# Optimization experiments

Measured on AMD Instinct MI355X. Metric: run time of the kernel, lower is better.

## Reference

```python
import jax, jax.numpy as jnp
import numpy as np

V, C, S, H, B, T = 10000, 1024, 128, 256, 16, 128
NEG = -1e10


def _mlp(x, w1, b1, w2, b2, wo, bo):
    # ResidualLayer (dropout=0, eval): relu(lin1) -> relu(lin2 + residual), then final Linear
    h = jax.nn.relu(x @ w1 + b1)
    h = jax.nn.relu(h @ w2 + b2 + x)
    return h @ wo + bo


def setup_inputs() -> dict:
    key = jax.random.key(0)
    ks = iter(jax.random.split(key, 32))
    d = {}
    d["text"] = jax.random.randint(next(ks), (B, T), 0, V)
    d["word2state"] = jax.random.randint(next(ks), (V, S), 0, C)

    def rn(shape, scale):
        return jax.random.normal(next(ks), shape, dtype=jnp.float32) * scale

    s = 1.0 / np.sqrt(H)
    d["start_emb"] = rn((C, H), 1.0)
    d["start_w1"], d["start_b1"] = rn((H, H), s), jnp.zeros((H,), jnp.float32)
    d["start_w2"], d["start_b2"] = rn((H, H), s), jnp.zeros((H,), jnp.float32)
    d["start_wo"], d["start_bo"] = rn((H, 1), s), jnp.zeros((1,), jnp.float32)
    d["state_emb"] = rn((C, H), 1.0)
    d["trans_w1"], d["trans_b1"] = rn((H, H), s), jnp.zeros((H,), jnp.float32)
    d["trans_w2"], d["trans_b2"] = rn((H, H), s), jnp.zeros((H,), jnp.float32)
    d["trans_wo"], d["trans_bo"] = rn((H, C), s), jnp.zeros((C,), jnp.float32)
    d["pre_emb"] = rn((C, H), 1.0)
    d["term_w1"], d["term_b1"] = rn((H, H), s), jnp.zeros((H,), jnp.float32)
    d["term_w2"], d["term_b2"] = rn((H, H), s), jnp.zeros((H,), jnp.float32)
    d["term_wo"], d["term_bo"] = rn((H, V), s), jnp.zeros((V,), jnp.float32)
    return d


def _evidence(text, word2state,
              start_emb, start_w1, start_b1, start_w2, start_b2, start_wo, start_bo,
              state_emb, trans_w1, trans_b1, trans_w2, trans_b2, trans_wo, trans_bo,
              pre_emb, term_w1, term_b1, term_w2, term_b2, term_wo, term_bo):
    # start distribution over C states
    start = jax.nn.log_softmax(
        _mlp(start_emb, start_w1, start_b1, start_w2, start_b2, start_wo, start_bo)[:, 0])
    # transition [C, C]
    transition = jax.nn.log_softmax(
        _mlp(state_emb, trans_w1, trans_b1, trans_w2, trans_b2, trans_wo, trans_bo), axis=-1)
    # emission with sparse state->word mask (scatter of word2state)
    em_logits = _mlp(pre_emb, term_w1, term_b1, term_w2, term_b2, term_wo, term_bo)  # [C, V]
    a = jnp.repeat(jnp.arange(V), S)  # word index per (word, slot)
    mask = jnp.zeros((C, V), dtype=bool).at[word2state.reshape(-1), a].set(True)
    emission = jax.nn.log_softmax(jnp.where(mask, em_logits, NEG), axis=-1)  # [C, V]

    clamped = word2state[text]  # [B, T, S] states allowed per token
    init = start[clamped[:, 0]]  # [B, S]
    # transition restricted to clamped states: [B, T-1, S_prev, S_next]
    lp = transition[clamped[:, :-1, :, None], clamped[:, 1:, None, :]]
    obs = emission[clamped, text[:, :, None]]  # [B, T, S]
    lp = lp + obs[:, 1:, None, :]                     # emission of next token
    lp = lp.at[:, 0].add(init[:, :, None] + obs[:, 0, :, None])
    lp = jnp.swapaxes(lp, -1, -2)  # [B, T-1, S_next, S_prev]

    # forward algorithm (log-space scan)
    alpha = jax.nn.logsumexp(lp[:, 0], axis=-1)  # [B, S]
    pots = jnp.swapaxes(lp[:, 1:], 0, 1)  # [T-2, B, S, S]

    def step(a_prev, pot):
        return jax.nn.logsumexp(pot + a_prev[:, None, :], axis=-1), None

    alpha_T, _ = jax.lax.scan(step, alpha, pots)
    return jax.nn.logsumexp(alpha_T, axis=-1).sum()


def reference(text, word2state,
              start_emb, start_w1, start_b1, start_w2, start_b2, start_wo, start_bo,
              state_emb, trans_w1, trans_b1, trans_w2, trans_b2, trans_wo, trans_bo,
              pre_emb, term_w1, term_b1, term_w2, term_b2, term_wo, term_bo):
    return _evidence(text, word2state,
                     start_emb, start_w1, start_b1, start_w2, start_b2, start_wo, start_bo,
                     state_emb, trans_w1, trans_b1, trans_w2, trans_b2, trans_wo, trans_bo,
                     pre_emb, term_w1, term_b1, term_w2, term_b2, term_wo, term_bo)
```

## Files before the change

### kernel.cpp

```cpp
#include <hip/hip_runtime.h>
#include <hip/hip_bf16.h>

#define V 10000
#define VP 10112
#define C 1024
#define S 128
#define H 256
#define B 16
#define T 128
#define NR 64
#define CHUNK 158
#define LDK 40

typedef unsigned short u16;
typedef unsigned int u32;
typedef __bf16 bf16x8 __attribute__((ext_vector_type(8)));
typedef float f32x4 __attribute__((ext_vector_type(4)));

static __device__ __forceinline__ float bf2f(u16 x){ return __uint_as_float(((u32)x)<<16); }
static __device__ __forceinline__ u16 f2bf(float f){ u32 u=__float_as_uint(f); return (u16)((u + 0x7FFFu + ((u>>16)&1u))>>16); }

struct Cvt3 { const float* s0; const float* s1; const float* s2; u16* d0; u16* d1; u16* d2; };
__global__ __launch_bounds__(256) void k_cvt3(Cvt3 a){
  const float* s = (blockIdx.y==0)? a.s0 : (blockIdx.y==1)? a.s1 : a.s2;
  u16* d = (blockIdx.y==0)? a.d0 : (blockIdx.y==1)? a.d1 : a.d2;
  int i = (blockIdx.x*256 + threadIdx.x)*8;
  float4 x0 = *(const float4*)(s+i);
  float4 x1 = *(const float4*)(s+i+4);
  u16 h[8] = {f2bf(x0.x),f2bf(x0.y),f2bf(x0.z),f2bf(x0.w),f2bf(x1.x),f2bf(x1.y),f2bf(x1.z),f2bf(x1.w)};
  *(uint4*)(d+i) = *(uint4*)h;
}

__global__ __launch_bounds__(256) void k_transpose(const float* __restrict__ src, u16* __restrict__ dst, int N){
  __shared__ float tile[32][33];
  int v0 = blockIdx.x*32, k0 = blockIdx.y*32;
  int tx = threadIdx.x, ty = threadIdx.y;
  for (int i=0;i<32;i+=8){
    int k = k0+ty+i, v = v0+tx;
    tile[ty+i][tx] = (v < N) ? src[(size_t)k*N + v] : 0.f;
  }
  __syncthreads();
  for (int i=0;i<32;i+=8){
    int v = v0+ty+i, k = k0+tx;
    dst[(size_t)v*H + k] = f2bf(tile[tx][ty+i]);
  }
}

struct T6 { const float* s[6]; u16* d[6]; };
__global__ __launch_bounds__(256) void k_transpose6(T6 a){
  const float* src = a.s[blockIdx.z];
  u16* dst = a.d[blockIdx.z];
  __shared__ float tile[32][33];
  int v0 = blockIdx.x*32, k0 = blockIdx.y*32;
  int tx = threadIdx.x, ty = threadIdx.y;
  for (int i=0;i<32;i+=8){
    int k = k0+ty+i, v = v0+tx;
    tile[ty+i][tx] = src[(size_t)k*H + v];
  }
  __syncthreads();
  for (int i=0;i<32;i+=8){
    int v = v0+ty+i, k = k0+tx;
    dst[(size_t)v*H + k] = f2bf(tile[tx][ty+i]);
  }
}

struct M3 { const u16* A[3]; const u16* W[3]; const float* bias[3]; const u16* R[3]; u16* O[3]; };
template<int RESID>
__global__ __launch_bounds__(256) void k_mlpg(M3 a){
  const int z = blockIdx.z;
  const u16* A  = a.A[z];
  const u16* BT = a.W[z];
  const float* bias = a.bias[z];
  const u16* Rm = a.R[z];
  u16* O = a.O[z];
  __shared__ u16 As[128*LDK];
  __shared__ u16 Bs[128*LDK];
  const int tid = threadIdx.x;
  const int lane = tid & 63, wave = tid >> 6;
  const int wm = wave >> 1, wn = wave & 1;
  const int m0 = blockIdx.y * 128, n0 = blockIdx.x * 128;
  const int lr = lane & 15, lg = lane >> 4;
  f32x4 acc[4][4] = {};
  const int sr = tid >> 1, sh = (tid & 1) * 16;
  for (int ks = 0; ks < H; ks += 32){
    const u16* ga = A  + (size_t)(m0 + sr)*H + ks + sh;
    const u16* gb = BT + (size_t)(n0 + sr)*H + ks + sh;
    uint4 a0 = *(const uint4*)ga;
    uint4 a1 = *(const uint4*)(ga + 8);
    uint4 b0 = *(const uint4*)gb;
    uint4 b1 = *(const uint4*)(gb + 8);
    __syncthreads();
    *(uint4*)&As[sr*LDK + sh]     = a0;
    *(uint4*)&As[sr*LDK + sh + 8] = a1;
    *(uint4*)&Bs[sr*LDK + sh]     = b0;
    *(uint4*)&Bs[sr*LDK + sh + 8] = b1;
    __syncthreads();
    bf16x8 af[4], bfr[4];
    #pragma unroll
    for (int m=0;m<4;m++) af[m]  = *(const bf16x8*)&As[(wm*64 + m*16 + lr)*LDK + lg*8];
    #pragma unroll
    for (int n=0;n<4;n++) bfr[n] = *(const bf16x8*)&Bs[(wn*64 + n*16 + lr)*LDK + lg*8];
    #pragma unroll
    for (int m=0;m<4;m++)
      #pragma unroll
      for (int n=0;n<4;n++)
        acc[m][n] = __builtin_amdgcn_mfma_f32_16x16x32_bf16(af[m], bfr[n], acc[m][n], 0,0,0);
  }
  #pragma unroll
  for (int m=0;m<4;m++){
    int r_g = m0 + wm*64 + m*16 + lg*4;
    #pragma unroll
    for (int n=0;n<4;n++){
      int n_g = n0 + wn*64 + n*16 + lr;
      float bv = bias[n_g];
      #pragma unroll
      for (int reg=0; reg<4; reg++){
        int r = r_g + reg;
        float val = acc[m][n][reg] + bv;
        if (RESID) val += bf2f(Rm[(size_t)r*H + n_g]);
        val = fmaxf(val, 0.f);
        O[(size_t)r*H + n_g] = f2bf(val);
      }
    }
  }
}

__global__ __launch_bounds__(1024) void k_start(
    const u16* __restrict__ h2, const float* __restrict__ wo, const float* __restrict__ bo,
    float* __restrict__ start_lp){
  const int c = threadIdx.x;
  const int lane = c & 63, wid = c >> 6;
  __shared__ float red[16];
  __shared__ float Ms, Zs;
  float acc = bo[0];
  const u16* row = h2 + (size_t)c*H;
  for (int k=0;k<H;k+=8){
    uint4 hv = *(const uint4*)(row+k);
    float4 w0 = *(const float4*)(wo+k);
    float4 w1 = *(const float4*)(wo+k+4);
    acc = fmaf(bf2f((u16)(hv.x&0xFFFFu)), w0.x, acc);
    acc = fmaf(bf2f((u16)(hv.x>>16)),     w0.y, acc);
    acc = fmaf(bf2f((u16)(hv.y&0xFFFFu)), w0.z, acc);
    acc = fmaf(bf2f((u16)(hv.y>>16)),     w0.w, acc);
    acc = fmaf(bf2f((u16)(hv.z&0xFFFFu)), w1.x, acc);
    acc = fmaf(bf2f((u16)(hv.z>>16)),     w1.y, acc);
    acc = fmaf(bf2f((u16)(hv.w&0xFFFFu)), w1.z, acc);
    acc = fmaf(bf2f((u16)(hv.w>>16)),     w1.w, acc);
  }
  float m = acc;
  for (int o=1;o<64;o<<=1) m = fmaxf(m, __shfl_xor(m,o));
  if (lane==0) red[wid]=m;
  __syncthreads();
  if (c==0){ float t=red[0]; for(int i=1;i<16;i++) t=fmaxf(t,red[i]); Ms=t; }
  __syncthreads();
  float M = Ms;
  float e = expf(acc - M);
  float sum = e;
  for (int o=1;o<64;o<<=1) sum += __shfl_xor(sum,o);
  __syncthreads();
  if (lane==0) red[wid]=sum;
  __syncthreads();
  if (c==0){ float t=0.f; for(int i=0;i<16;i++) t+=red[i]; Zs=t; }
  __syncthreads();
  start_lp[c] = acc - (M + logf(Zs));
}

template<int BIAS_ROW, int BF16OUT>
__global__ __launch_bounds__(256) void k_gemm(
    const u16* __restrict__ A, const u16* __restrict__ BT,
    const float* __restrict__ bias, int biasBound,
    void* __restrict__ outp, int ldout){
  __shared__ u16 As[128*LDK];
  __shared__ u16 Bs[128*LDK];
  const int tid = threadIdx.x;
  const int lane = tid & 63, wave = tid >> 6;
  const int wm = wave >> 1, wn = wave & 1;
  const int m0 = blockIdx.y * 128, n0 = blockIdx.x * 128;
  const int lr = lane & 15, lg = lane >> 4;
  f32x4 acc[4][4] = {};
  const int sr = tid >> 1, sh = (tid & 1) * 16;
  for (int ks = 0; ks < H; ks += 32){
    const u16* ga = A  + (size_t)(m0 + sr)*H + ks + sh;
    const u16* gb = BT + (size_t)(n0 + sr)*H + ks + sh;
    uint4 a0 = *(const uint4*)ga;
    uint4 a1 = *(const uint4*)(ga + 8);
    uint4 b0 = *(const uint4*)gb;
    uint4 b1 = *(const uint4*)(gb + 8);
    __syncthreads();
    *(uint4*)&As[sr*LDK + sh]     = a0;
    *(uint4*)&As[sr*LDK + sh + 8] = a1;
    *(uint4*)&Bs[sr*LDK + sh]     = b0;
    *(uint4*)&Bs[sr*LDK + sh + 8] = b1;
    __syncthreads();
    bf16x8 af[4], bfr[4];
    #pragma unroll
    for (int m=0;m<4;m++) af[m]  = *(const bf16x8*)&As[(wm*64 + m*16 + lr)*LDK + lg*8];
    #pragma unroll
    for (int n=0;n<4;n++) bfr[n] = *(const bf16x8*)&Bs[(wn*64 + n*16 + lr)*LDK + lg*8];
    #pragma unroll
    for (int m=0;m<4;m++)
      #pragma unroll
      for (int n=0;n<4;n++)
        acc[m][n] = __builtin_amdgcn_mfma_f32_16x16x32_bf16(af[m], bfr[n], acc[m][n], 0,0,0);
  }
  #pragma unroll
  for (int m=0;m<4;m++){
    int r_g = m0 + wm*64 + m*16 + lg*4;
    #pragma unroll
    for (int n=0;n<4;n++){
      int n_g = n0 + wn*64 + n*16 + lr;
      float bcol = BIAS_ROW ? 0.f : bias[n_g];
      #pragma unroll
      for (int reg=0; reg<4; reg++){
        int r = r_g + reg;
        float bv = BIAS_ROW ? ((r < biasBound) ? bias[r] : 0.f) : bcol;
        float val = acc[m][n][reg] + bv;
        if (BF16OUT) ((u16*)outp)[(size_t)r*ldout + n_g] = f2bf(val);
        else         ((float*)outp)[(size_t)r*ldout + n_g] = val;
      }
    }
  }
}

__global__ __launch_bounds__(256) void k_softmax(const float* __restrict__ TL, u16* __restrict__ P){
  const int c = blockIdx.x;
  const int tid = threadIdx.x, lane = tid & 63, wid = tid >> 6;
  __shared__ float red[4];
  __shared__ float Ms, Zs;
  float4 v = ((const float4*)(TL + (size_t)c*C))[tid];
  float m = fmaxf(fmaxf(v.x,v.y), fmaxf(v.z,v.w));
  for (int o=1;o<64;o<<=1) m = fmaxf(m, __shfl_xor(m,o));
  if (lane==0) red[wid] = m;
  __syncthreads();
  if (tid==0) Ms = fmaxf(fmaxf(red[0],red[1]), fmaxf(red[2],red[3]));
  __syncthreads();
  float M = Ms;
  float e0 = expf(v.x-M), e1 = expf(v.y-M), e2 = expf(v.z-M), e3 = expf(v.w-M);
  float s = (e0+e1)+(e2+e3);
  for (int o=1;o<64;o<<=1) s += __shfl_xor(s,o);
  if (lane==0) red[wid] = s;
  __syncthreads();
  if (tid==0) Zs = red[0]+red[1]+red[2]+red[3];
  __syncthreads();
  float inv = 1.f/Zs;
  u32 lo = (u32)f2bf(e0*inv) | ((u32)f2bf(e1*inv)<<16);
  u32 hi = (u32)f2bf(e2*inv) | ((u32)f2bf(e3*inv)<<16);
  *(uint2*)(P + (size_t)c*C + tid*4) = make_uint2(lo, hi);
}

__global__ __launch_bounds__(256) void k_colmax(const u16* __restrict__ EM, float* __restrict__ shiftp){
  const int c = blockIdx.x*256 + threadIdx.x;
  const int v0 = blockIdx.y*CHUNK;
  float m = -1e30f;
  const u16* p = EM + (size_t)v0*C + c;
  #pragma unroll 2
  for (int i=0;i<CHUNK;i++){ m = fmaxf(m, bf2f(p[0])); p += C; }
  shiftp[(size_t)blockIdx.y*C + c] = m;
}

__global__ void k_shiftc(const float* __restrict__ shiftp, float* __restrict__ shift){
  int c = threadIdx.x + blockIdx.x*blockDim.x;
  if (c < C){
    float m = -1e30f;
    for (int r=0;r<NR;r++) m = fmaxf(m, shiftp[(size_t)r*C + c]);
    shift[c] = m;
  }
}

__global__ __launch_bounds__(256) void k_scatter(
    const int* __restrict__ w2s, const u16* __restrict__ EM,
    const float* __restrict__ shift, u16* __restrict__ D){
  int idx = blockIdx.x*256 + threadIdx.x;
  int v = idx >> 7;
  const int c = w2s[idx];
  float val = bf2f(EM[(size_t)v*C + c]);
  D[(size_t)v*C + c] = f2bf(expf(val - shift[c]));
}

__global__ __launch_bounds__(256) void k_colsum(const u16* __restrict__ D, float* __restrict__ sumexp){
  const int c = blockIdx.x*256 + threadIdx.x;
  const int v0 = blockIdx.y*CHUNK;
  float s = 0.f;
  const u16* p = D + (size_t)v0*C + c;
  #pragma unroll 2
  for (int i=0;i<CHUNK;i++){ s += bf2f(p[0]); p += C; }
  sumexp[(size_t)blockIdx.y*C + c] = s;
}

__global__ void k_lse(const float* __restrict__ shift, const float* __restrict__ sumexp, float* __restrict__ lse){
  int c = threadIdx.x + blockIdx.x*blockDim.x;
  if (c < C){
    float s = 0.f;
    for (int r=0;r<NR;r++) s += sumexp[(size_t)r*C + c];
    lse[c] = shift[c] + logf(s);
  }
}

__global__ __launch_bounds__(128) void k_obs(
    const int* __restrict__ text, const int* __restrict__ w2s,
    const u16* __restrict__ EM, const float* __restrict__ lse,
    float* __restrict__ obs){
  const int bt = blockIdx.x;
  const int s = threadIdx.x;
  const int v = text[bt];
  const int c = w2s[(size_t)v*S + s];
  obs[(size_t)bt*S + s] = bf2f(EM[(size_t)v*C + c]) - lse[c];
}

__global__ __launch_bounds__(256) void k_pot(
    const int* __restrict__ text, const int* __restrict__ w2s,
    const float* __restrict__ start_lp, const float* __restrict__ obs,
    const u16* __restrict__ P, u16* __restrict__ pot){
  const int t = blockIdx.x;
  const int b = blockIdx.y;
  const int tid = threadIdx.x;
  u16* dst = pot + ((size_t)b*128 + t)*(S*S);
  if (t == 127){
    #pragma unroll
    for (int k=0;k<8;k++){
      int e0 = (k*256 + tid)*8;
      int row = e0>>7, c0 = e0&127;
      union { uint4 w; u16 h[8]; } u;
      u.w = make_uint4(0,0,0,0);
      int d = row - c0;
      if (d >= 0 && d < 8) u.h[d] = 0x3F80u;
      *(uint4*)(dst + e0) = u.w;
    }
    return;
  }
  __shared__ int cp[S], cn[S];
  __shared__ float eo[S];
  __shared__ float a0[S];
  __shared__ u32 tileW[S*65];
  u16* tile16 = (u16*)tileW;
  if (tid < 128){
    int cpv = w2s[(size_t)text[b*T + t]*S + tid];
    cp[tid] = cpv;
    a0[tid] = (t==0) ? expf(start_lp[cpv] + obs[(size_t)(b*T)*S + tid]) : 1.0f;
    eo[tid] = expf(obs[((size_t)b*T + t + 1)*S + tid]);
  } else {
    cn[tid-128] = w2s[(size_t)text[b*T + t+1]*S + (tid-128)];
  }
  __syncthreads();
  const int sp_half = tid >> 7;
  const int sn = tid & 127;
  const int cnv = cn[sn];
  const float eov = eo[sn];
  for (int it=0; it<64; ++it){
    int sp = it*2 + sp_half;
    tile16[sn*130 + sp] = f2bf(bf2f(P[(size_t)cp[sp]*C + cnv]) * eov * a0[sp]);
  }
  __syncthreads();
  if (t & 1){
    #pragma unroll
    for (int ii=0; ii<8; ++ii){
      int i0 = (ii*256 + tid)*8;
      int sn2 = i0>>7, sp2 = i0&127;
      const u32* tw = tileW + sn2*65 + (sp2>>1);
      uint4 w4; w4.x = tw[0]; w4.y = tw[1]; w4.z = tw[2]; w4.w = tw[3];
      *(uint4*)(dst + i0) = w4;
    }
  } else {
    #pragma unroll
    for (int ii=0; ii<8; ++ii){
      int i0 = (ii*256 + tid)*8;
      int sp2 = i0>>7, sn0 = i0&127;
      union { uint4 w; u16 h[8]; } u;
      #pragma unroll
      for (int j=0;j<8;j++) u.h[j] = tile16[(sn0+j)*130 + sp2];
      *(uint4*)(dst + i0) = u.w;
    }
  }
}

__global__ __launch_bounds__(256) void k_pair(
    const u16* __restrict__ in, u16* __restrict__ out,
    float* __restrict__ scales, int nin, int soff){
  const int j = blockIdx.x;
  const int b = blockIdx.y;
  const int nout = nin >> 1;
  const u16* Ag = in + ((size_t)b*nin + 2*j+1)*(S*S);
  const u16* Bg = in + ((size_t)b*nin + 2*j  )*(S*S);
  u16* Cg = out + ((size_t)b*nout + j)*(S*S);
  const int tid = threadIdx.x;
  const int lane = tid & 63, wave = tid >> 6;
  const int wm = wave >> 1, wn = wave & 1;
  const int lr = lane & 15, lg = lane >> 4;
  f32x4 acc[4][4] = {};
  #pragma unroll
  for (int kc=0; kc<4; ++kc){
    bf16x8 af[4], bfr[4];
    #pragma unroll
    for (int m=0;m<4;m++) af[m]  = *(const bf16x8*)(Ag + (size_t)(wm*64+m*16+lr)*128 + kc*32 + lg*8);
    #pragma unroll
    for (int n=0;n<4;n++) bfr[n] = *(const bf16x8*)(Bg + (size_t)(wn*64+n*16+lr)*128 + kc*32 + lg*8);
    #pragma unroll
    for (int m=0;m<4;m++)
      #pragma unroll
      for (int n=0;n<4;n++)
        acc[m][n] = __builtin_amdgcn_mfma_f32_16x16x32_bf16(af[m], bfr[n], acc[m][n], 0,0,0);
  }
  __shared__ float red[4];
  float mx = 0.f;
  #pragma unroll
  for (int m=0;m<4;m++)
    #pragma unroll
    for (int n=0;n<4;n++)
      #pragma unroll
      for (int r=0;r<4;r++) mx = fmaxf(mx, acc[m][n][r]);
  for (int o=1;o<64;o<<=1) mx = fmaxf(mx, __shfl_xor(mx,o));
  if (lane==0) red[wave] = mx;
  __syncthreads();
  mx = fmaxf(fmaxf(red[0],red[1]), fmaxf(red[2],red[3]));
  const float sc = 1.0f / mx;
  if (tid==0) scales[(size_t)b*127 + soff + j] = logf(mx);
  if (j & 1){
    #pragma unroll
    for (int m=0;m<4;m++){
      int rg = wm*64 + m*16 + lg*4;
      #pragma unroll
      for (int n=0;n<4;n++){
        int cg = wn*64 + n*16 + lr;
        #pragma unroll
        for (int r=0;r<4;r++) Cg[(size_t)(rg+r)*128 + cg] = f2bf(acc[m][n][r]*sc);
      }
    }
  } else {
    #pragma unroll
    for (int m=0;m<4;m++){
      int rg = wm*64 + m*16 + lg*4;
      #pragma unroll
      for (int n=0;n<4;n++){
        int cg = wn*64 + n*16 + lr;
        float v0=acc[m][n][0]*sc, v1=acc[m][n][1]*sc, v2=acc[m][n][2]*sc, v3=acc[m][n][3]*sc;
        u32 p0, p1;
        asm("v_cvt_pk_bf16_f32 %0, %1, %2" : "=v"(p0) : "v"(v0), "v"(v1));
        asm("v_cvt_pk_bf16_f32 %0, %1, %2" : "=v"(p1) : "v"(v2), "v"(v3));
        *(uint2*)(Cg + (size_t)cg*128 + rg) = make_uint2(p0, p1);
      }
    }
  }
}

__global__ __launch_bounds__(256) void k_fin(
    const u16* __restrict__ fin, const float* __restrict__ scales, float* __restrict__ res){
  const int b = blockIdx.x;
  const int tid = threadIdx.x, lane = tid & 63, wid = tid >> 6;
  __shared__ float red[8];
  const u16* p = fin + (size_t)b*(S*S);
  float s = 0.f;
  #pragma unroll
  for (int i=0;i<8;i++){
    uint4 w = *(const uint4*)(p + (i*256+tid)*8);
    s += bf2f((u16)(w.x&0xFFFFu)) + bf2f((u16)(w.x>>16))
       + bf2f((u16)(w.y&0xFFFFu)) + bf2f((u16)(w.y>>16))
       + bf2f((u16)(w.z&0xFFFFu)) + bf2f((u16)(w.z>>16))
       + bf2f((u16)(w.w&0xFFFFu)) + bf2f((u16)(w.w>>16));
  }
  for (int o=1;o<64;o<<=1) s += __shfl_xor(s,o);
  if (lane==0) red[wid] = s;
  float sl = (tid < 127) ? scales[(size_t)b*127 + tid] : 0.f;
  for (int o=1;o<64;o<<=1) sl += __shfl_xor(sl,o);
  if (lane==0) red[4+wid] = sl;
  __syncthreads();
  if (tid==0){
    float tot = red[0]+red[1]+red[2]+red[3];
    float ssum = red[4]+red[5]+red[6]+red[7];
    res[b] = logf(tot) + ssum;
  }
}

__global__ void k_final(const float* __restrict__ res, float* __restrict__ out){
  if (threadIdx.x==0){
    float s = 0.f;
    for (int i=0;i<B;i++) s += res[i];
    out[0] = s;
  }
}

extern "C" void kernel_launch(void* const* d_in, const int* in_sizes, int n_in,
                              void* d_out, int out_size, void* d_ws, size_t ws_size,
                              hipStream_t stream){
  const int*   text      = (const int*)d_in[0];
  const int*   w2s       = (const int*)d_in[1];
  const float* start_emb = (const float*)d_in[2];
  const float* start_w1  = (const float*)d_in[3];
  const float* start_b1  = (const float*)d_in[4];
  const float* start_w2  = (const float*)d_in[5];
  const float* start_b2  = (const float*)d_in[6];
  const float* start_wo  = (const float*)d_in[7];
  const float* start_bo  = (const float*)d_in[8];
  const float* state_emb = (const float*)d_in[9];
  const float* trans_w1  = (const float*)d_in[10];
  const float* trans_b1  = (const float*)d_in[11];
  const float* trans_w2  = (const float*)d_in[12];
  const float* trans_b2  = (const float*)d_in[13];
  const float* trans_wo  = (const float*)d_in[14];
  const float* trans_bo  = (const float*)d_in[15];
  const float* pre_emb   = (const float*)d_in[16];
  const float* term_w1   = (const float*)d_in[17];
  const float* term_b1   = (const float*)d_in[18];
  const float* term_w2   = (const float*)d_in[19];
  const float* term_b2   = (const float*)d_in[20];
  const float* term_wo   = (const float*)d_in[21];
  const float* term_bo   = (const float*)d_in[22];

  char* ws = (char*)d_ws;
  size_t off = 0;
  auto alloc = [&](size_t bytes)->char*{ char* p = ws + off; off += (bytes + 255) & ~(size_t)255; return p; };
  u16*   embb     = (u16*)  alloc(sizeof(u16)*3*(size_t)C*H);
  u16*   h1b      = (u16*)  alloc(sizeof(u16)*3*(size_t)C*H);
  u16*   h2b      = (u16*)  alloc(sizeof(u16)*3*(size_t)C*H);
  u16*   wt       = (u16*)  alloc(sizeof(u16)*6*(size_t)H*H);
  float* start_lp = (float*)alloc(sizeof(float)*C);
  float* shift    = (float*)alloc(sizeof(float)*C);
  float* shiftp   = (float*)alloc(sizeof(float)*(size_t)C*NR);
  float* sumexp   = (float*)alloc(sizeof(float)*(size_t)C*NR);
  float* lse      = (float*)alloc(sizeof(float)*C);
  float* resb     = (float*)alloc(sizeof(float)*B);
  float* scales   = (float*)alloc(sizeof(float)*(size_t)B*127);
  u16*   P        = (u16*)  alloc(sizeof(u16)*(size_t)C*C);
  u16*   wotb     = (u16*)  alloc(sizeof(u16)*(size_t)VP*H);
  u16*   wottr    = (u16*)  alloc(sizeof(u16)*(size_t)C*H);
  float* obs      = (float*)alloc(sizeof(float)*(size_t)B*T*S);
  u16*   potS     = (u16*)  alloc(sizeof(u16)*(size_t)B*128*S*S);
  u16*   treeA    = (u16*)  alloc(sizeof(u16)*(size_t)B*64*S*S);
  u16*   treeB    = (u16*)  alloc(sizeof(u16)*(size_t)B*32*S*S);
  u16*   EM       = (u16*)potS;
  float* TL       = (float*)treeA;
  u16*   D        = (u16*)((char*)treeA + sizeof(float)*(size_t)C*C);
  (void)ws_size; (void)in_sizes; (void)n_in; (void)out_size;

  u16* embb0 = embb, *embb1 = embb + (size_t)C*H, *embb2 = embb + 2*(size_t)C*H;
  u16* h1b0 = h1b, *h1b1 = h1b + (size_t)C*H, *h1b2 = h1b + 2*(size_t)C*H;
  u16* h2b0 = h2b, *h2b1 = h2b + (size_t)C*H, *h2b2 = h2b + 2*(size_t)C*H;

  hipMemsetAsync(D, 0, sizeof(u16)*(size_t)VP*C, stream);

  Cvt3 cv; cv.s0 = start_emb; cv.s1 = state_emb; cv.s2 = pre_emb;
  cv.d0 = embb0; cv.d1 = embb1; cv.d2 = embb2;
  k_cvt3<<<dim3(C*H/(256*8), 3), dim3(256), 0, stream>>>(cv);

  T6 t6;
  t6.s[0]=start_w1; t6.s[1]=start_w2; t6.s[2]=trans_w1; t6.s[3]=trans_w2; t6.s[4]=term_w1; t6.s[5]=term_w2;
  for (int i=0;i<6;i++) t6.d[i] = wt + (size_t)i*H*H;
  k_transpose6<<<dim3(H/32, H/32, 6), dim3(32,8), 0, stream>>>(t6);

  M3 l1;
  l1.A[0]=embb0; l1.A[1]=embb1; l1.A[2]=embb2;
  l1.W[0]=wt;    l1.W[1]=wt+2*(size_t)H*H; l1.W[2]=wt+4*(size_t)H*H;
  l1.bias[0]=start_b1; l1.bias[1]=trans_b1; l1.bias[2]=term_b1;
  l1.R[0]=l1.R[1]=l1.R[2]=nullptr;
  l1.O[0]=h1b0; l1.O[1]=h1b1; l1.O[2]=h1b2;
  k_mlpg<0><<<dim3(H/128, C/128, 3), dim3(256), 0, stream>>>(l1);

  M3 l2;
  l2.A[0]=h1b0; l2.A[1]=h1b1; l2.A[2]=h1b2;
  l2.W[0]=wt+(size_t)H*H; l2.W[1]=wt+3*(size_t)H*H; l2.W[2]=wt+5*(size_t)H*H;
  l2.bias[0]=start_b2; l2.bias[1]=trans_b2; l2.bias[2]=term_b2;
  l2.R[0]=embb0; l2.R[1]=embb1; l2.R[2]=embb2;
  l2.O[0]=h2b0; l2.O[1]=h2b1; l2.O[2]=h2b2;
  k_mlpg<1><<<dim3(H/128, C/128, 3), dim3(256), 0, stream>>>(l2);

  k_start<<<dim3(1), dim3(1024), 0, stream>>>(h2b0, start_wo, start_bo, start_lp);
  k_transpose<<<dim3(VP/32, H/32), dim3(32,8), 0, stream>>>(term_wo, wotb, V);
  k_transpose<<<dim3(C/32, H/32), dim3(32,8), 0, stream>>>(trans_wo, wottr, C);
  k_gemm<0,0><<<dim3(C/128, C/128), dim3(256), 0, stream>>>(h2b1, wottr, trans_bo, C, TL, C);
  k_softmax<<<dim3(C), dim3(256), 0, stream>>>(TL, P);
  k_gemm<1,1><<<dim3(C/128, VP/128), dim3(256), 0, stream>>>(wotb, h2b2, term_bo, V, EM, C);
  k_colmax<<<dim3(C/256, NR), dim3(256), 0, stream>>>(EM, shiftp);
  k_shiftc<<<dim3((C+255)/256), dim3(256), 0, stream>>>(shiftp, shift);
  k_scatter<<<dim3(V*S/256), dim3(256), 0, stream>>>(w2s, EM, shift, D);
  k_colsum<<<dim3(C/256, NR), dim3(256), 0, stream>>>(D, sumexp);
  k_lse<<<dim3((C+255)/256), dim3(256), 0, stream>>>(shift, sumexp, lse);
  k_obs<<<dim3(B*T), dim3(128), 0, stream>>>(text, w2s, EM, lse, obs);
  k_pot<<<dim3(128, B), dim3(256), 0, stream>>>(text, w2s, start_lp, obs, P, potS);

  {
    u16* lin = potS;
    u16* bufs[2] = { treeA, treeB };
    int nin = 128, soff = 0, cur = 0;
    while (nin > 1){
      int nout = nin >> 1;
      k_pair<<<dim3(nout, B), dim3(256), 0, stream>>>(lin, bufs[cur], scales, nin, soff);
      lin = bufs[cur];
      cur ^= 1;
      soff += nout;
      nin = nout;
    }
    k_fin<<<dim3(B), dim3(256), 0, stream>>>(lin, scales, resb);
  }
  k_final<<<dim3(1), dim3(64), 0, stream>>>(resb, (float*)d_out);
}
```

Measured before the change: 294.1 us.

## Fuse potential construction into first pairwise product and column-max into emission GEMM

```diff
diff --git a/kernel.cpp b/kernel.cpp
--- a/kernel.cpp
+++ b/kernel.cpp
@@ -10,7 +10,9 @@
 #define T 128
 #define NR 64
 #define CHUNK 158
+#define NRP 158
 #define LDK 40
+#define PITCH 136
 
 typedef unsigned short u16;
 typedef unsigned int u32;
@@ -165,11 +167,11 @@
   start_lp[c] = acc - (M + logf(Zs));
 }
 
-template<int BIAS_ROW, int BF16OUT>
+template<int BIAS_ROW, int BF16OUT, int COLMAX>
 __global__ __launch_bounds__(256) void k_gemm(
     const u16* __restrict__ A, const u16* __restrict__ BT,
     const float* __restrict__ bias, int biasBound,
-    void* __restrict__ outp, int ldout){
+    void* __restrict__ outp, int ldout, float* __restrict__ cmax){
   __shared__ u16 As[128*LDK];
   __shared__ u16 Bs[128*LDK];
   const int tid = threadIdx.x;
@@ -203,6 +205,7 @@
       for (int n=0;n<4;n++)
         acc[m][n] = __builtin_amdgcn_mfma_f32_16x16x32_bf16(af[m], bfr[n], acc[m][n], 0,0,0);
   }
+  float cmx[4] = {-1e30f,-1e30f,-1e30f,-1e30f};
   #pragma unroll
   for (int m=0;m<4;m++){
     int r_g = m0 + wm*64 + m*16 + lg*4;
@@ -215,9 +218,19 @@
         int r = r_g + reg;
         float bv = BIAS_ROW ? ((r < biasBound) ? bias[r] : 0.f) : bcol;
         float val = acc[m][n][reg] + bv;
+        if (COLMAX) cmx[n] = fmaxf(cmx[n], val);
         if (BF16OUT) ((u16*)outp)[(size_t)r*ldout + n_g] = f2bf(val);
         else         ((float*)outp)[(size_t)r*ldout + n_g] = val;
       }
+    }
+  }
+  if (COLMAX){
+    #pragma unroll
+    for (int n=0;n<4;n++){
+      float m_ = cmx[n];
+      m_ = fmaxf(m_, __shfl_xor(m_,16));
+      m_ = fmaxf(m_, __shfl_xor(m_,32));
+      if (lg==0) cmax[((size_t)(blockIdx.y*2 + wm))*C + n0 + wn*64 + n*16 + lr] = m_;
     }
   }
 }
@@ -248,21 +261,11 @@
   *(uint2*)(P + (size_t)c*C + tid*4) = make_uint2(lo, hi);
 }
 
-__global__ __launch_bounds__(256) void k_colmax(const u16* __restrict__ EM, float* __restrict__ shiftp){
-  const int c = blockIdx.x*256 + threadIdx.x;
-  const int v0 = blockIdx.y*CHUNK;
-  float m = -1e30f;
-  const u16* p = EM + (size_t)v0*C + c;
-  #pragma unroll 2
-  for (int i=0;i<CHUNK;i++){ m = fmaxf(m, bf2f(p[0])); p += C; }
-  shiftp[(size_t)blockIdx.y*C + c] = m;
-}
-
 __global__ void k_shiftc(const float* __restrict__ shiftp, float* __restrict__ shift){
   int c = threadIdx.x + blockIdx.x*blockDim.x;
   if (c < C){
     float m = -1e30f;
-    for (int r=0;r<NR;r++) m = fmaxf(m, shiftp[(size_t)r*C + c]);
+    for (int r=0;r<NRP;r++) m = fmaxf(m, shiftp[(size_t)r*C + c]);
     shift[c] = m;
   }
 }
@@ -307,68 +310,110 @@
   obs[(size_t)bt*S + s] = bf2f(EM[(size_t)v*C + c]) - lse[c];
 }
 
-__global__ __launch_bounds__(256) void k_pot(
+__global__ __launch_bounds__(256) void k_pair0(
     const int* __restrict__ text, const int* __restrict__ w2s,
     const float* __restrict__ start_lp, const float* __restrict__ obs,
-    const u16* __restrict__ P, u16* __restrict__ pot){
-  const int t = blockIdx.x;
+    const u16* __restrict__ P, u16* __restrict__ out, float* __restrict__ scales){
+  const int j = blockIdx.x;
   const int b = blockIdx.y;
+  const int t0 = 2*j, t1 = 2*j+1;
+  __shared__ __align__(16) u16 tA[128*PITCH];
+  __shared__ __align__(16) u16 tB[128*PITCH];
+  __shared__ int cp0[S], cn0[S], cp1[S], cn1[S];
+  __shared__ float eo0[S], eo1[S], a00[S];
+  __shared__ float red[4];
   const int tid = threadIdx.x;
-  u16* dst = pot + ((size_t)b*128 + t)*(S*S);
-  if (t == 127){
-    #pragma unroll
-    for (int k=0;k<8;k++){
-      int e0 = (k*256 + tid)*8;
-      int row = e0>>7, c0 = e0&127;
-      union { uint4 w; u16 h[8]; } u;
-      u.w = make_uint4(0,0,0,0);
-      int d = row - c0;
-      if (d >= 0 && d < 8) u.h[d] = 0x3F80u;
-      *(uint4*)(dst + e0) = u.w;
-    }
-    return;
-  }
-  __shared__ int cp[S], cn[S];
-  __shared__ float eo[S];
-  __shared__ float a0[S];
-  __shared__ u32 tileW[S*65];
-  u16* tile16 = (u16*)tileW;
   if (tid < 128){
-    int cpv = w2s[(size_t)text[b*T + t]*S + tid];
-    cp[tid] = cpv;
-    a0[tid] = (t==0) ? expf(start_lp[cpv] + obs[(size_t)(b*T)*S + tid]) : 1.0f;
-    eo[tid] = expf(obs[((size_t)b*T + t + 1)*S + tid]);
+    int s = tid;
+    int cpv = w2s[(size_t)text[b*T + t0]*S + s];
+    cp0[s] = cpv;
+    cn0[s] = w2s[(size_t)text[b*T + t0+1]*S + s];
+    eo0[s] = expf(obs[((size_t)b*T + t0 + 1)*S + s]);
+    a00[s] = (t0==0) ? expf(start_lp[cpv] + obs[(size_t)(b*T)*S + s]) : 1.0f;
+  } else if (t1 < 127){
+    int s = tid-128;
+    cp1[s] = w2s[(size_t)text[b*T + t1]*S + s];
+    cn1[s] = w2s[(size_t)text[b*T + t1+1]*S + s];
+    eo1[s] = expf(obs[((size_t)b*T + t1 + 1)*S + s]);
+  }
+  __syncthreads();
+  const int sn = tid & 127, half = tid >> 7;
+  {
+    const float e = eo0[sn];
+    for (int it=0; it<64; ++it){
+      int sp = it*2 + half;
+      float v = bf2f(P[(size_t)cp0[sp]*C + cn0[sn]]) * e * a00[sp];
+      tB[sp*PITCH + sn] = f2bf(v);
+    }
+  }
+  if (t1 < 127){
+    const float e = eo1[sn];
+    for (int it=0; it<64; ++it){
+      int sp = it*2 + half;
+      tA[sn*PITCH + sp] = f2bf(bf2f(P[(size_t)cp1[sp]*C + cn1[sn]]) * e);
+    }
   } else {
-    cn[tid-128] = w2s[(size_t)text[b*T + t+1]*S + (tid-128)];
-  }
-  __syncthreads();
-  const int sp_half = tid >> 7;
-  const int sn = tid & 127;
-  const int cnv = cn[sn];
-  const float eov = eo[sn];
-  for (int it=0; it<64; ++it){
-    int sp = it*2 + sp_half;
-    tile16[sn*130 + sp] = f2bf(bf2f(P[(size_t)cp[sp]*C + cnv]) * eov * a0[sp]);
-  }
-  __syncthreads();
-  if (t & 1){
-    #pragma unroll
-    for (int ii=0; ii<8; ++ii){
-      int i0 = (ii*256 + tid)*8;
-      int sn2 = i0>>7, sp2 = i0&127;
-      const u32* tw = tileW + sn2*65 + (sp2>>1);
-      uint4 w4; w4.x = tw[0]; w4.y = tw[1]; w4.z = tw[2]; w4.w = tw[3];
-      *(uint4*)(dst + i0) = w4;
+    for (int it=0; it<64; ++it){
+      int sp = it*2 + half;
+      tA[sn*PITCH + sp] = (sn==sp) ? (u16)0x3F80u : (u16)0u;
+    }
+  }
+  __syncthreads();
+  const int lane = tid & 63, wave = tid >> 6;
+  const int wm = wave >> 1, wn = wave & 1;
+  const int lr = lane & 15, lg = lane >> 4;
+  f32x4 acc[4][4] = {};
+  #pragma unroll
+  for (int kc=0; kc<4; ++kc){
+    bf16x8 af[4], bfr[4];
+    #pragma unroll
+    for (int m=0;m<4;m++) af[m]  = *(const bf16x8*)&tA[(wm*64+m*16+lr)*PITCH + kc*32 + lg*8];
+    #pragma unroll
+    for (int n=0;n<4;n++) bfr[n] = *(const bf16x8*)&tB[(wn*64+n*16+lr)*PITCH + kc*32 + lg*8];
+    #pragma unroll
+    for (int m=0;m<4;m++)
+      #pragma unroll
+      for (int n=0;n<4;n++)
+        acc[m][n] = __builtin_amdgcn_mfma_f32_16x16x32_bf16(af[m], bfr[n], acc[m][n], 0,0,0);
+  }
+  float mx = 0.f;
+  #pragma unroll
+  for (int m=0;m<4;m++)
+    #pragma unroll
+    for (int n=0;n<4;n++)
+      #pragma unroll
+      for (int r=0;r<4;r++) mx = fmaxf(mx, acc[m][n][r]);
+  for (int o=1;o<64;o<<=1) mx = fmaxf(mx, __shfl_xor(mx,o));
+  if (lane==0) red[wave] = mx;
+  __syncthreads();
+  mx = fmaxf(fmaxf(red[0],red[1]), fmaxf(red[2],red[3]));
+  const float sc = 1.0f / mx;
+  if (tid==0) scales[(size_t)b*127 + j] = logf(mx);
+  u16* Cg = out + ((size_t)b*64 + j)*(S*S);
+  if (j & 1){
+    #pragma unroll
+    for (int m=0;m<4;m++){
+      int rg = wm*64 + m*16 + lg*4;
+      #pragma unroll
+      for (int n=0;n<4;n++){
+        int cg = wn*64 + n*16 + lr;
+        #pragma unroll
+        for (int r=0;r<4;r++) Cg[(size_t)(rg+r)*128 + cg] = f2bf(acc[m][n][r]*sc);
+      }
     }
   } else {
     #pragma unroll
-    for (int ii=0; ii<8; ++ii){
-      int i0 = (ii*256 + tid)*8;
-      int sp2 = i0>>7, sn0 = i0&127;
-      union { uint4 w; u16 h[8]; } u;
-      #pragma unroll
-      for (int j=0;j<8;j++) u.h[j] = tile16[(sn0+j)*130 + sp2];
-      *(uint4*)(dst + i0) = u.w;
+    for (int m=0;m<4;m++){
+      int rg = wm*64 + m*16 + lg*4;
+      #pragma unroll
+      for (int n=0;n<4;n++){
+        int cg = wn*64 + n*16 + lr;
+        float v0=acc[m][n][0]*sc, v1=acc[m][n][1]*sc, v2=acc[m][n][2]*sc, v3=acc[m][n][3]*sc;
+        u32 p0, p1;
+        asm("v_cvt_pk_bf16_f32 %0, %1, %2" : "=v"(p0) : "v"(v0), "v"(v1));
+        asm("v_cvt_pk_bf16_f32 %0, %1, %2" : "=v"(p1) : "v"(v2), "v"(v3));
+        *(uint2*)(Cg + (size_t)cg*128 + rg) = make_uint2(p0, p1);
+      }
     }
   }
 }
@@ -514,7 +559,7 @@
   u16*   wt       = (u16*)  alloc(sizeof(u16)*6*(size_t)H*H);
   float* start_lp = (float*)alloc(sizeof(float)*C);
   float* shift    = (float*)alloc(sizeof(float)*C);
-  float* shiftp   = (float*)alloc(sizeof(float)*(size_t)C*NR);
+  float* shiftp   = (float*)alloc(sizeof(float)*(size_t)C*NRP);
   float* sumexp   = (float*)alloc(sizeof(float)*(size_t)C*NR);
   float* lse      = (float*)alloc(sizeof(float)*C);
   float* resb     = (float*)alloc(sizeof(float)*B);
@@ -523,10 +568,9 @@
   u16*   wotb     = (u16*)  alloc(sizeof(u16)*(size_t)VP*H);
   u16*   wottr    = (u16*)  alloc(sizeof(u16)*(size_t)C*H);
   float* obs      = (float*)alloc(sizeof(float)*(size_t)B*T*S);
-  u16*   potS     = (u16*)  alloc(sizeof(u16)*(size_t)B*128*S*S);
+  u16*   EM       = (u16*)  alloc(sizeof(u16)*(size_t)VP*C);
   u16*   treeA    = (u16*)  alloc(sizeof(u16)*(size_t)B*64*S*S);
   u16*   treeB    = (u16*)  alloc(sizeof(u16)*(size_t)B*32*S*S);
-  u16*   EM       = (u16*)potS;
   float* TL       = (float*)treeA;
   u16*   D        = (u16*)((char*)treeA + sizeof(float)*(size_t)C*C);
   (void)ws_size; (void)in_sizes; (void)n_in; (void)out_size;
@@ -565,21 +609,21 @@
   k_start<<<dim3(1), dim3(1024), 0, stream>>>(h2b0, start_wo, start_bo, start_lp);
   k_transpose<<<dim3(VP/32, H/32), dim3(32,8), 0, stream>>>(term_wo, wotb, V);
   k_transpose<<<dim3(C/32, H/32), dim3(32,8), 0, stream>>>(trans_wo, wottr, C);
-  k_gemm<0,0><<<dim3(C/128, C/128), dim3(256), 0, stream>>>(h2b1, wottr, trans_bo, C, TL, C);
+  k_gemm<0,0,0><<<dim3(C/128, C/128), dim3(256), 0, stream>>>(h2b1, wottr, trans_bo, C, TL, C, nullptr);
   k_softmax<<<dim3(C), dim3(256), 0, stream>>>(TL, P);
-  k_gemm<1,1><<<dim3(C/128, VP/128), dim3(256), 0, stream>>>(wotb, h2b2, term_bo, V, EM, C);
-  k_colmax<<<dim3(C/256, NR), dim3(256), 0, stream>>>(EM, shiftp);
+  k_gemm<1,1,1><<<dim3(C/128, VP/128), dim3(256), 0, stream>>>(wotb, h2b2, term_bo, V, EM, C, shiftp);
   k_shiftc<<<dim3((C+255)/256), dim3(256), 0, stream>>>(shiftp, shift);
   k_scatter<<<dim3(V*S/256), dim3(256), 0, stream>>>(w2s, EM, shift, D);
   k_colsum<<<dim3(C/256, NR), dim3(256), 0, stream>>>(D, sumexp);
   k_lse<<<dim3((C+255)/256), dim3(256), 0, stream>>>(shift, sumexp, lse);
   k_obs<<<dim3(B*T), dim3(128), 0, stream>>>(text, w2s, EM, lse, obs);
-  k_pot<<<dim3(128, B), dim3(256), 0, stream>>>(text, w2s, start_lp, obs, P, potS);
+
+  k_pair0<<<dim3(64, B), dim3(256), 0, stream>>>(text, w2s, start_lp, obs, P, treeA, scales);
 
   {
-    u16* lin = potS;
-    u16* bufs[2] = { treeA, treeB };
-    int nin = 128, soff = 0, cur = 0;
+    u16* lin = treeA;
+    u16* bufs[2] = { treeB, treeA };
+    int nin = 64, soff = 64, cur = 0;
     while (nin > 1){
       int nout = nin >> 1;
       k_pair<<<dim3(nout, B), dim3(256), 0, stream>>>(lin, bufs[cur], scales, nin, soff);
```

After: 280.2 us. -4.7%, faster.
